# Optimization experiments

Measured on AMD Instinct MI355X. Metric: run time of the kernel, lower is better.

Reference implementation:

```python
import jax, jax.numpy as jnp
import numpy as np

N_HEADS = 8
HEAD_DIM = 64  # hidden_dim 512 / 8 heads
EPS = 1e-12    # F.normalize clamp_min eps


def setup_inputs() -> dict:
    key = jax.random.key(0)
    k1, k2, k3, k4 = jax.random.split(key, 4)
    B, C, H, W = 2, 256, 48, 48
    hidden = N_HEADS * HEAD_DIM
    x = jax.random.normal(k1, (B, C, H, W), dtype=jnp.float32)
    w_qkv = jax.random.normal(k2, (hidden * 3, C), dtype=jnp.float32) * 0.02
    w_proj = jax.random.normal(k3, (C, hidden), dtype=jnp.float32) * 0.02
    b_proj = jax.random.normal(k4, (C,), dtype=jnp.float32) * 0.02
    return {"x": x, "w_qkv": w_qkv, "w_proj": w_proj, "b_proj": b_proj}


def _l2norm_tokens(t):
    # normalize along the token axis (last dim), matching F.normalize(dim=-1)
    n = jnp.sqrt(jnp.sum(t * t, axis=-1, keepdims=True))
    return t / jnp.maximum(n, EPS)


def reference(x, w_qkv, w_proj, b_proj):
    B, C, H, W = x.shape
    N = H * W
    # 1x1 conv == channel matmul
    qkv = jnp.einsum('oc,bchw->bohw', w_qkv, x)  # [B, 3*hidden, H, W]
    qkv = qkv.reshape(B, 3, N_HEADS, HEAD_DIM, N)
    q, k, v = qkv[:, 0], qkv[:, 1], qkv[:, 2]    # each [B, h, d, N]
    q = _l2norm_tokens(q)
    k = _l2norm_tokens(k)
    # attn = q^T @ k over head_dim -> [B, h, N, N]; note: qk_scale unused in source
    attn = jnp.einsum('bhdn,bhdm->bhnm', q, k)
    attn = jax.nn.softmax(attn, axis=-1)
    # out = attn @ v^T -> [B, h, N, d], then permute to [B, h, d, N]
    out = jnp.einsum('bhnm,bhdm->bhdn', attn, v)
    out = out.reshape(B, N_HEADS * HEAD_DIM, H, W)
    # proj 1x1 conv with bias
    y = jnp.einsum('oc,bchw->bohw', w_proj, out) + b_proj[None, :, None, None]
    return y
```

## Files before the change

kernel.cpp:

```cpp
#include <hip/hip_runtime.h>
#include <math.h>

#define NTOK 2304
#define BATCH 2
#define CIN 256
#define HID 512
#define NH 8
#define LOG2E 1.44269504088896340736f

typedef __attribute__((ext_vector_type(8))) short bfrag;
typedef __attribute__((ext_vector_type(16))) float f32x16;

#if __has_builtin(__builtin_amdgcn_exp2f)
#define EXP2(x) __builtin_amdgcn_exp2f(x)
#else
#define EXP2(x) exp2f(x)
#endif

__device__ __forceinline__ unsigned f2bf(float f) {
    unsigned u = __float_as_uint(f);
    u += 0x7FFF + ((u >> 16) & 1);
    return u >> 16;
}

__device__ __forceinline__ unsigned pk_trunc(float a, float b) {
    return __builtin_amdgcn_perm(__float_as_uint(b), __float_as_uint(a), 0x07060302u);
}

__device__ __forceinline__ void softmax_frag(
    const f32x16& accS, int h, float& ps0, float& ps1, bfrag& P0, bfrag& P1)
{
    unsigned dw[8];
#pragma unroll
    for (int i = 0; i < 8; i++) {
        float plo = EXP2(accS[2 * i]);
        float phi = EXP2(accS[2 * i + 1]);
        dw[i] = pk_trunc(plo, phi);
        ps0 += __uint_as_float(dw[i] << 16);
        ps1 += __uint_as_float(dw[i] & 0xffff0000u);
    }
    unsigned sa0 = h ? dw[0] : dw[2], sb0 = h ? dw[1] : dw[3];
    unsigned sa1 = h ? dw[4] : dw[6], sb1 = h ? dw[5] : dw[7];
    unsigned ra0 = (unsigned)__shfl_xor((int)sa0, 32, 64);
    unsigned rb0 = (unsigned)__shfl_xor((int)sb0, 32, 64);
    unsigned ra1 = (unsigned)__shfl_xor((int)sa1, 32, 64);
    unsigned rb1 = (unsigned)__shfl_xor((int)sb1, 32, 64);
    union { bfrag f; unsigned u[4]; } U0, U1;
    U0.u[0] = h ? ra0 : dw[0];  U0.u[1] = h ? rb0 : dw[1];
    U0.u[2] = h ? dw[2] : ra0;  U0.u[3] = h ? dw[3] : rb0;
    U1.u[0] = h ? ra1 : dw[4];  U1.u[1] = h ? rb1 : dw[5];
    U1.u[2] = h ? dw[6] : ra1;  U1.u[3] = h ? dw[7] : rb1;
    P0 = U0.f; P1 = U1.f;
}

__global__ __launch_bounds__(256) void pack_weights(
    const float* __restrict__ wq, short* __restrict__ wqb,
    const float* __restrict__ wp, short* __restrict__ wpb,
    float* __restrict__ sumsq)
{
    if (blockIdx.x == 0) {
        ((float4*)sumsq)[threadIdx.x * 2] = make_float4(0.f, 0.f, 0.f, 0.f);
        ((float4*)sumsq)[threadIdx.x * 2 + 1] = make_float4(0.f, 0.f, 0.f, 0.f);
    }
    int e = (blockIdx.x * 256 + threadIdx.x) * 8;
    const int NQ = 1536 * 256;
    const float* src; short* dst;
    if (e < NQ) {
        int row = e >> 8, c = e & 255;
        int off = (((row >> 5) * 16 + (c >> 4)) * 64 + ((c >> 3) & 1) * 32 + (row & 31)) * 8;
        src = wq + e; dst = wqb + off;
    } else {
        int e2 = e - NQ;
        int row = e2 >> 9, c = e2 & 511;
        int off = (((row >> 5) * 32 + (c >> 4)) * 64 + ((c >> 3) & 1) * 32 + (row & 31)) * 8;
        src = wp + e2; dst = wpb + off;
    }
    float4 v0 = ((const float4*)src)[0];
    float4 v1 = ((const float4*)src)[1];
    unsigned b0 = f2bf(v0.x) | (f2bf(v0.y) << 16);
    unsigned b1 = f2bf(v0.z) | (f2bf(v0.w) << 16);
    unsigned b2 = f2bf(v1.x) | (f2bf(v1.y) << 16);
    unsigned b3 = f2bf(v1.z) | (f2bf(v1.w) << 16);
    *((uint4*)dst) = make_uint4(b0, b1, b2, b3);
}

__global__ __launch_bounds__(256) void pack_xT(
    const float* __restrict__ x, short* __restrict__ xT)
{
    int n0 = blockIdx.x * 64, c0 = blockIdx.y * 64, b = blockIdx.z;
    __shared__ float sT[64][65];
    int tid = threadIdx.x, lane = tid & 63, wv = tid >> 6;
    for (int c = wv; c < 64; c += 4)
        sT[c][lane] = x[((size_t)b * CIN + c0 + c) * NTOK + n0 + lane];
    __syncthreads();
    int n = tid >> 2, c4 = (tid & 3) * 16;
    unsigned buf[8];
#pragma unroll
    for (int i = 0; i < 8; i++)
        buf[i] = f2bf(sT[c4 + 2 * i][n]) | (f2bf(sT[c4 + 2 * i + 1][n]) << 16);
    int n_tok = n0 + n;
    int l31n = n & 31;
    short* dst = xT + (((size_t)b * 72 + (n_tok >> 5)) * 16 + ((c0 + c4) >> 4)) * 512;
    ((uint4*)(dst + (0 * 32 + l31n) * 8))[0] = make_uint4(buf[0], buf[1], buf[2], buf[3]);
    ((uint4*)(dst + (1 * 32 + l31n) * 8))[0] = make_uint4(buf[4], buf[5], buf[6], buf[7]);
}

__global__ __launch_bounds__(256, 2) void gemm_qkv(
    const short* __restrict__ A,
    const short* __restrict__ B,
    short* __restrict__ qku,
    short* __restrict__ vb,
    float* __restrict__ sumsq)
{
    int b = blockIdx.z;
    int o0 = blockIdx.y * 128;
    int n0 = blockIdx.x * 128;
    int tid = threadIdx.x, wv = tid >> 6, lane = tid & 63;
    int h = lane >> 5, l31 = lane & 31;

    const short* pa = A + ((size_t)(o0 >> 5) * 16) * 512 + lane * 8;
    const short* pb = B + (((size_t)b * 72 + (n0 >> 5) + wv) * 16) * 512 + lane * 8;

    f32x16 acc[4];
#pragma unroll
    for (int rb = 0; rb < 4; rb++)
#pragma unroll
        for (int r = 0; r < 16; r++) acc[rb][r] = 0.f;

#pragma unroll 2
    for (int kc = 0; kc < 16; kc++) {
        bfrag a0 = *(const bfrag*)(pa + (size_t)(0 * 16 + kc) * 512);
        bfrag a1 = *(const bfrag*)(pa + (size_t)(1 * 16 + kc) * 512);
        bfrag a2 = *(const bfrag*)(pa + (size_t)(2 * 16 + kc) * 512);
        bfrag a3 = *(const bfrag*)(pa + (size_t)(3 * 16 + kc) * 512);
        bfrag bb = *(const bfrag*)(pb + (size_t)kc * 512);
        acc[0] = __builtin_amdgcn_mfma_f32_32x32x16_bf16(a0, bb, acc[0], 0, 0, 0);
        acc[1] = __builtin_amdgcn_mfma_f32_32x32x16_bf16(a1, bb, acc[1], 0, 0, 0);
        acc[2] = __builtin_amdgcn_mfma_f32_32x32x16_bf16(a2, bb, acc[2], 0, 0, 0);
        acc[3] = __builtin_amdgcn_mfma_f32_32x32x16_bf16(a3, bb, acc[3], 0, 0, 0);
    }

    int nn = n0 + wv * 32 + l31;
    if (o0 < 1024) {
        int sel = o0 >> 9;
        short* Qb = qku + (size_t)sel * (16 * NTOK * 64);
        int mbase = (nn >> 5) * 4, tl = nn & 31;
#pragma unroll
        for (int rb = 0; rb < 4; rb++)
#pragma unroll
            for (int r = 0; r < 16; r++) {
                int ml = (r & 3) + 8 * (r >> 2) + 4 * h;
                int o = o0 + rb * 32 + ml;
                int hh2 = (o >> 6) & 7, d = o & 63;
                float v = acc[rb][r];
                float sq = v * v;
#pragma unroll
                for (int off = 1; off < 32; off <<= 1)
                    sq += __shfl_xor(sq, off, 64);
                if (l31 == 0)
                    atomicAdd(sumsq + b * 1024 + o, sq);
                Qb[(size_t)(b * 8 + hh2) * (NTOK * 64)
                   + (size_t)(mbase + (d >> 4)) * 512
                   + (((d >> 3) & 1) * 32 + tl) * 8 + (d & 7)] = (short)f2bf(v);
            }
    } else {
        short* V = vb + (size_t)b * 512 * NTOK;
        int ov = o0 - 1024;
        int mb = nn >> 5, jc = (nn >> 4) & 1, hv = (nn >> 3) & 1, e = nn & 7;
#pragma unroll
        for (int rb = 0; rb < 4; rb++)
#pragma unroll
            for (int r = 0; r < 16; r++) {
                int ml = (r & 3) + 8 * (r >> 2) + 4 * h;
                int row = ov + rb * 32 + ml;
                int hh2 = row >> 6, dl = row & 63;
                int jr = dl >> 5, l31v = dl & 31;
                V[((((size_t)hh2 * 72 + mb) * 4 + jr * 2 + jc) * 64
                   + hv * 32 + l31v) * 8 + e] = (short)f2bf(acc[rb][r]);
            }
    }
}

__global__ __launch_bounds__(256) void scale_qk(
    short* __restrict__ qkt, const float* __restrict__ sumsq)
{
    int s = blockIdx.x * 256 + threadIdx.x;
    int lane = s & 63;
    int rest = s >> 6;
    int fi = rest & 3;
    int selbh = rest / 288;
    int sel = selbh >> 4, bh = selbh & 15;
    int b = bh >> 3, hh = bh & 7;
    int d0 = fi * 16 + (lane >> 5) * 8;
    const float* sp = sumsq + b * 1024 + sel * 512 + hh * 64 + d0;
    float scl = sel == 0 ? LOG2E : 1.f;
    float4 s0 = ((const float4*)sp)[0];
    float4 s1 = ((const float4*)sp)[1];
    float i0 = scl / fmaxf(sqrtf(s0.x), 1e-12f);
    float i1 = scl / fmaxf(sqrtf(s0.y), 1e-12f);
    float i2 = scl / fmaxf(sqrtf(s0.z), 1e-12f);
    float i3 = scl / fmaxf(sqrtf(s0.w), 1e-12f);
    float i4 = scl / fmaxf(sqrtf(s1.x), 1e-12f);
    float i5 = scl / fmaxf(sqrtf(s1.y), 1e-12f);
    float i6 = scl / fmaxf(sqrtf(s1.z), 1e-12f);
    float i7 = scl / fmaxf(sqrtf(s1.w), 1e-12f);
    uint4 v = ((uint4*)qkt)[s];
    unsigned o0w = f2bf(__uint_as_float(v.x << 16) * i0)
                 | (f2bf(__uint_as_float(v.x & 0xffff0000u) * i1) << 16);
    unsigned o1w = f2bf(__uint_as_float(v.y << 16) * i2)
                 | (f2bf(__uint_as_float(v.y & 0xffff0000u) * i3) << 16);
    unsigned o2w = f2bf(__uint_as_float(v.z << 16) * i4)
                 | (f2bf(__uint_as_float(v.z & 0xffff0000u) * i5) << 16);
    unsigned o3w = f2bf(__uint_as_float(v.w << 16) * i6)
                 | (f2bf(__uint_as_float(v.w & 0xffff0000u) * i7) << 16);
    ((uint4*)qkt)[s] = make_uint4(o0w, o1w, o2w, o3w);
}

__global__ __launch_bounds__(256, 4) void attn_nb(
    const short* __restrict__ qkt,
    const short* __restrict__ vb,
    short* __restrict__ Opart,
    float* __restrict__ lsum)
{
    int bid = blockIdx.x;
    int g = bid & 63;
    int bh = g >> 2, ms = g & 3;
    int ntile = bid >> 6;
    int b = bh >> 3, hh = bh & 7;
    int tid = threadIdx.x, wv = tid >> 6, lane = tid & 63;
    int h = lane >> 5, l31 = lane & 31;
    int nb = ntile * 128 + wv * 32;
    int mb0 = ms * 18;

    const short* Qt = qkt + (size_t)bh * NTOK * 64;
    const short* kp = qkt + (size_t)16 * NTOK * 64 + (size_t)bh * NTOK * 64
                    + ((size_t)mb0 * 4) * 512 + lane * 8;
    const short* vp = vb + (((size_t)(b * 8 + hh) * 72 + mb0) * 4) * 512 + lane * 8;

    bfrag bQ[4];
    {
        const short* q0 = Qt + ((size_t)(nb >> 5) * 4) * 512 + lane * 8;
#pragma unroll
        for (int i = 0; i < 4; i++) bQ[i] = *(const bfrag*)(q0 + i * 512);
    }

    f32x16 aL, aH;
#pragma unroll
    for (int r = 0; r < 16; r++) { aL[r] = 0.f; aH[r] = 0.f; }
    float s0 = 0.f, s1 = 0.f;

    bfrag ck[4], cv[4];
#pragma unroll
    for (int i = 0; i < 4; i++) {
        ck[i] = *(const bfrag*)(kp + i * 512);
        cv[i] = *(const bfrag*)(vp + i * 512);
    }

#pragma unroll 2
    for (int it = 0; it < 18; it++) {
        kp += 2048; vp += 2048;
        bfrag nk[4], nv[4];
#pragma unroll
        for (int i = 0; i < 4; i++) {
            nk[i] = *(const bfrag*)(kp + i * 512);
            nv[i] = *(const bfrag*)(vp + i * 512);
        }

        bfrag P0, P1;
        {
            f32x16 accS;
#pragma unroll
            for (int r = 0; r < 16; r++) accS[r] = 0.f;
            accS = __builtin_amdgcn_mfma_f32_32x32x16_bf16(ck[0], bQ[0], accS, 0, 0, 0);
            accS = __builtin_amdgcn_mfma_f32_32x32x16_bf16(ck[1], bQ[1], accS, 0, 0, 0);
            accS = __builtin_amdgcn_mfma_f32_32x32x16_bf16(ck[2], bQ[2], accS, 0, 0, 0);
            accS = __builtin_amdgcn_mfma_f32_32x32x16_bf16(ck[3], bQ[3], accS, 0, 0, 0);
            softmax_frag(accS, h, s0, s1, P0, P1);
        }
        aL = __builtin_amdgcn_mfma_f32_32x32x16_bf16(P0, cv[0], aL, 0, 0, 0);
        aL = __builtin_amdgcn_mfma_f32_32x32x16_bf16(P1, cv[1], aL, 0, 0, 0);
        aH = __builtin_amdgcn_mfma_f32_32x32x16_bf16(P0, cv[2], aH, 0, 0, 0);
        aH = __builtin_amdgcn_mfma_f32_32x32x16_bf16(P1, cv[3], aH, 0, 0, 0);

#pragma unroll
        for (int i = 0; i < 4; i++) { ck[i] = nk[i]; cv[i] = nv[i]; }
    }

    float p0 = s0 + s1;
    p0 += __shfl_xor(p0, 32, 64);
    if (h == 0)
        lsum[((size_t)ms * 16 + bh) * NTOK + nb + l31] = p0;

    short* Ob = Opart + (size_t)ms * (2ull * NTOK * HID)
              + (size_t)b * NTOK * HID + hh * 64;
#pragma unroll
    for (int r = 0; r < 16; r++) {
        int ml = (r & 3) + 8 * (r >> 2) + 4 * h;
        Ob[(size_t)(nb + ml) * HID + l31] = (short)f2bf(aL[r]);
        Ob[(size_t)(nb + ml) * HID + 32 + l31] = (short)f2bf(aH[r]);
    }
}

__global__ __launch_bounds__(256) void combine(
    const short* __restrict__ Opart, const float* __restrict__ lsum,
    short* __restrict__ aoT)
{
    int s = blockIdx.x * 256 + threadIdx.x;
    int lane = s & 63, kc = (s >> 6) & 31, nbb = s >> 11;
    int b = nbb >= 72 ? 1 : 0, nb = nbb - 72 * b;
    int h = lane >> 5, l31 = lane & 31;
    int n = nb * 32 + l31;
    int k0 = kc * 16 + h * 8;
    int hh = kc >> 2;
    float l = 0.f;
#pragma unroll
    for (int ms = 0; ms < 4; ms++)
        l += lsum[((size_t)ms * 16 + b * 8 + hh) * NTOK + n];
    float inv = 1.f / l;
    float a[8] = {0.f, 0.f, 0.f, 0.f, 0.f, 0.f, 0.f, 0.f};
#pragma unroll
    for (int ms = 0; ms < 4; ms++) {
        const short* P = Opart + (size_t)ms * (2ull * NTOK * HID)
                       + ((size_t)b * NTOK + n) * HID + k0;
        uint4 v = *(const uint4*)P;
        a[0] += __uint_as_float(v.x << 16);
        a[1] += __uint_as_float(v.x & 0xffff0000u);
        a[2] += __uint_as_float(v.y << 16);
        a[3] += __uint_as_float(v.y & 0xffff0000u);
        a[4] += __uint_as_float(v.z << 16);
        a[5] += __uint_as_float(v.z & 0xffff0000u);
        a[6] += __uint_as_float(v.w << 16);
        a[7] += __uint_as_float(v.w & 0xffff0000u);
    }
    unsigned b0 = f2bf(a[0] * inv) | (f2bf(a[1] * inv) << 16);
    unsigned b1 = f2bf(a[2] * inv) | (f2bf(a[3] * inv) << 16);
    unsigned b2 = f2bf(a[4] * inv) | (f2bf(a[5] * inv) << 16);
    unsigned b3 = f2bf(a[6] * inv) | (f2bf(a[7] * inv) << 16);
    *((uint4*)(aoT + (size_t)s * 8)) = make_uint4(b0, b1, b2, b3);
}

__global__ __launch_bounds__(256, 2) void gemm_proj(
    const short* __restrict__ A,
    const short* __restrict__ B,
    const float* __restrict__ bias, float* __restrict__ y)
{
    int b = blockIdx.z;
    int o0 = blockIdx.y * 64;
    int n0 = blockIdx.x * 128;
    int tid = threadIdx.x, wv = tid >> 6, lane = tid & 63;
    int h = lane >> 5, l31 = lane & 31;

    const short* pa = A + ((size_t)(o0 >> 5) * 32) * 512 + lane * 8;
    const short* pb = B + (((size_t)b * 72 + (n0 >> 5) + wv) * 32) * 512 + lane * 8;

    f32x16 acc0, acc1;
#pragma unroll
    for (int r = 0; r < 16; r++) { acc0[r] = 0.f; acc1[r] = 0.f; }

#pragma unroll 4
    for (int kc = 0; kc < 32; kc++) {
        bfrag a0 = *(const bfrag*)(pa + (size_t)kc * 512);
        bfrag a1 = *(const bfrag*)(pa + (size_t)(32 + kc) * 512);
        bfrag bb = *(const bfrag*)(pb + (size_t)kc * 512);
        acc0 = __builtin_amdgcn_mfma_f32_32x32x16_bf16(a0, bb, acc0, 0, 0, 0);
        acc1 = __builtin_amdgcn_mfma_f32_32x32x16_bf16(a1, bb, acc1, 0, 0, 0);
    }

    int nn = n0 + wv * 32 + l31;
#pragma unroll
    for (int r = 0; r < 16; r++) {
        int ml = (r & 3) + 8 * (r >> 2) + 4 * h;
        y[((size_t)b * CIN + o0 + ml) * NTOK + nn] = acc0[r] + bias[o0 + ml];
        y[((size_t)b * CIN + o0 + 32 + ml) * NTOK + nn] = acc1[r] + bias[o0 + 32 + ml];
    }
}

extern "C" void kernel_launch(void* const* d_in, const int* in_sizes, int n_in,
                              void* d_out, int out_size, void* d_ws, size_t ws_size,
                              hipStream_t stream)
{
    const float* x      = (const float*)d_in[0];
    const float* w_qkv  = (const float*)d_in[1];
    const float* w_proj = (const float*)d_in[2];
    const float* b_proj = (const float*)d_in[3];
    float* y = (float*)d_out;

    short* Opart = (short*)d_ws;
    short* vb    = (short*)((char*)d_ws + 18874368);
    short* qkt   = (short*)((char*)d_ws + 23592960);
    short* aoT   = (short*)((char*)d_ws + 23592960);
    float* lsum  = (float*)((char*)d_ws + 33030144);
    short* xT    = (short*)((char*)d_ws + 33030144);
    short* wqb   = (short*)((char*)d_ws + 35389440);
    short* wpb   = (short*)((char*)d_ws + 36175872);
    float* sumsq = (float*)((char*)d_ws + 36438016);

    pack_weights<<<(1536 * 256 + 256 * 512) / 8 / 256, 256, 0, stream>>>(
        w_qkv, wqb, w_proj, wpb, sumsq);
    pack_xT<<<dim3(NTOK / 64, CIN / 64, BATCH), 256, 0, stream>>>(x, xT);
    gemm_qkv<<<dim3(NTOK / 128, 1536 / 128, BATCH), 256, 0, stream>>>(
        wqb, xT, qkt, vb, sumsq);
    scale_qk<<<2304, 256, 0, stream>>>(qkt, sumsq);
    attn_nb<<<1152, 256, 0, stream>>>(qkt, vb, Opart, lsum);
    combine<<<1152, 256, 0, stream>>>(Opart, lsum, aoT);
    gemm_proj<<<dim3(NTOK / 128, CIN / 64, BATCH), 256, 0, stream>>>(
        wpb, aoT, b_proj, y);
}
```

Before: 163.0 us.

## Split sumsq into own kernel, double query tiles per wave, retile Opart layout

Removes the per-element shuffle reduction and atomics from the QKV GEMM epilogue and moves the squared-norm accumulation into a separate sumsq_qk kernel that reads the bf16 q/k buffer. The attention kernel now processes two 32-query tiles per wave with 128-thread blocks, so each K/V fragment load feeds twice the MFMA work at the cost of more accumulator registers. Opart is written in the fragment-tiled layout the combine kernel reads linearly, which simplifies combine's addressing. The softmax row-sum accumulation is rebalanced into a tree to shorten the dependency chain. Norms are now computed from bf16-rounded values instead of fp32, a small numerical change.

```diff
diff --git a/kernel.cpp b/kernel.cpp
--- a/kernel.cpp
+++ b/kernel.cpp
@@ -23,6 +23,10 @@
     return u >> 16;
 }
 
+__device__ __forceinline__ float bf2f(unsigned short s) {
+    return __uint_as_float(((unsigned)s) << 16);
+}
+
 __device__ __forceinline__ unsigned pk_trunc(float a, float b) {
     return __builtin_amdgcn_perm(__float_as_uint(b), __float_as_uint(a), 0x07060302u);
 }
@@ -31,14 +35,17 @@
     const f32x16& accS, int h, float& ps0, float& ps1, bfrag& P0, bfrag& P1)
 {
     unsigned dw[8];
+    float e0[8], e1[8];
 #pragma unroll
     for (int i = 0; i < 8; i++) {
         float plo = EXP2(accS[2 * i]);
         float phi = EXP2(accS[2 * i + 1]);
         dw[i] = pk_trunc(plo, phi);
-        ps0 += __uint_as_float(dw[i] << 16);
-        ps1 += __uint_as_float(dw[i] & 0xffff0000u);
-    }
+        e0[i] = __uint_as_float(dw[i] << 16);
+        e1[i] = __uint_as_float(dw[i] & 0xffff0000u);
+    }
+    ps0 += ((e0[0] + e0[1]) + (e0[2] + e0[3])) + ((e0[4] + e0[5]) + (e0[6] + e0[7]));
+    ps1 += ((e1[0] + e1[1]) + (e1[2] + e1[3])) + ((e1[4] + e1[5]) + (e1[6] + e1[7]));
     unsigned sa0 = h ? dw[0] : dw[2], sb0 = h ? dw[1] : dw[3];
     unsigned sa1 = h ? dw[4] : dw[6], sb1 = h ? dw[5] : dw[7];
     unsigned ra0 = (unsigned)__shfl_xor((int)sa0, 32, 64);
@@ -109,8 +116,7 @@
     const short* __restrict__ A,
     const short* __restrict__ B,
     short* __restrict__ qku,
-    short* __restrict__ vb,
-    float* __restrict__ sumsq)
+    short* __restrict__ vb)
 {
     int b = blockIdx.z;
     int o0 = blockIdx.y * 128;
@@ -152,16 +158,9 @@
                 int ml = (r & 3) + 8 * (r >> 2) + 4 * h;
                 int o = o0 + rb * 32 + ml;
                 int hh2 = (o >> 6) & 7, d = o & 63;
-                float v = acc[rb][r];
-                float sq = v * v;
-#pragma unroll
-                for (int off = 1; off < 32; off <<= 1)
-                    sq += __shfl_xor(sq, off, 64);
-                if (l31 == 0)
-                    atomicAdd(sumsq + b * 1024 + o, sq);
                 Qb[(size_t)(b * 8 + hh2) * (NTOK * 64)
                    + (size_t)(mbase + (d >> 4)) * 512
-                   + (((d >> 3) & 1) * 32 + tl) * 8 + (d & 7)] = (short)f2bf(v);
+                   + (((d >> 3) & 1) * 32 + tl) * 8 + (d & 7)] = (short)f2bf(acc[rb][r]);
             }
     } else {
         short* V = vb + (size_t)b * 512 * NTOK;
@@ -178,6 +177,41 @@
                 V[((((size_t)hh2 * 72 + mb) * 4 + jr * 2 + jc) * 64
                    + hv * 32 + l31v) * 8 + e] = (short)f2bf(acc[rb][r]);
             }
+    }
+}
+
+__global__ __launch_bounds__(64) void sumsq_qk(
+    const short* __restrict__ qkt, float* __restrict__ sumsq)
+{
+    int bid = blockIdx.x;
+    int mc = bid % 9;
+    int rest = bid / 9;
+    int i = rest & 3;
+    int selbh = rest >> 2;
+    int lane = threadIdx.x;
+    const short* p = qkt + (((size_t)selbh * 72 + mc * 8) * 4 + i) * 512 + lane * 8;
+    float sq[8] = {0.f, 0.f, 0.f, 0.f, 0.f, 0.f, 0.f, 0.f};
+#pragma unroll
+    for (int m = 0; m < 8; m++) {
+        bfrag v = *(const bfrag*)(p + (size_t)m * 2048);
+#pragma unroll
+        for (int e = 0; e < 8; e++) {
+            float f = bf2f((unsigned short)v[e]);
+            sq[e] += f * f;
+        }
+    }
+#pragma unroll
+    for (int off = 1; off <= 16; off <<= 1)
+#pragma unroll
+        for (int e = 0; e < 8; e++)
+            sq[e] += __shfl_xor(sq[e], off, 64);
+    if ((lane & 31) == 0) {
+        int sel = selbh >> 4, bh = selbh & 15;
+        int b = bh >> 3, hh = bh & 7, hsel = lane >> 5;
+        int dbase = i * 16 + hsel * 8;
+        float* dst = sumsq + b * 1024 + sel * 512 + hh * 64 + dbase;
+#pragma unroll
+        for (int e = 0; e < 8; e++) atomicAdd(dst + e, sq[e]);
     }
 }
 
@@ -216,7 +250,7 @@
     ((uint4*)qkt)[s] = make_uint4(o0w, o1w, o2w, o3w);
 }
 
-__global__ __launch_bounds__(256, 4) void attn_nb(
+__global__ __launch_bounds__(128, 2) void attn_nb(
     const short* __restrict__ qkt,
     const short* __restrict__ vb,
     short* __restrict__ Opart,
@@ -229,7 +263,8 @@
     int b = bh >> 3, hh = bh & 7;
     int tid = threadIdx.x, wv = tid >> 6, lane = tid & 63;
     int h = lane >> 5, l31 = lane & 31;
-    int nb = ntile * 128 + wv * 32;
+    int nb0 = ntile * 128 + wv * 32;
+    int nb1 = nb0 + 64;
     int mb0 = ms * 18;
 
     const short* Qt = qkt + (size_t)bh * NTOK * 64;
@@ -237,17 +272,21 @@
                     + ((size_t)mb0 * 4) * 512 + lane * 8;
     const short* vp = vb + (((size_t)(b * 8 + hh) * 72 + mb0) * 4) * 512 + lane * 8;
 
-    bfrag bQ[4];
+    bfrag bQ0[4], bQ1[4];
     {
-        const short* q0 = Qt + ((size_t)(nb >> 5) * 4) * 512 + lane * 8;
-#pragma unroll
-        for (int i = 0; i < 4; i++) bQ[i] = *(const bfrag*)(q0 + i * 512);
-    }
-
-    f32x16 aL, aH;
-#pragma unroll
-    for (int r = 0; r < 16; r++) { aL[r] = 0.f; aH[r] = 0.f; }
-    float s0 = 0.f, s1 = 0.f;
+        const short* q0 = Qt + ((size_t)(nb0 >> 5) * 4) * 512 + lane * 8;
+        const short* q1 = Qt + ((size_t)(nb1 >> 5) * 4) * 512 + lane * 8;
+#pragma unroll
+        for (int i = 0; i < 4; i++) {
+            bQ0[i] = *(const bfrag*)(q0 + i * 512);
+            bQ1[i] = *(const bfrag*)(q1 + i * 512);
+        }
+    }
+
+    f32x16 aL0, aH0, aL1, aH1;
+#pragma unroll
+    for (int r = 0; r < 16; r++) { aL0[r] = 0.f; aH0[r] = 0.f; aL1[r] = 0.f; aH1[r] = 0.f; }
+    float s00 = 0.f, s01 = 0.f, s10 = 0.f, s11 = 0.f;
 
     bfrag ck[4], cv[4];
 #pragma unroll
@@ -266,38 +305,63 @@
             nv[i] = *(const bfrag*)(vp + i * 512);
         }
 
-        bfrag P0, P1;
+        bfrag P00, P01, P10, P11;
         {
             f32x16 accS;
 #pragma unroll
             for (int r = 0; r < 16; r++) accS[r] = 0.f;
-            accS = __builtin_amdgcn_mfma_f32_32x32x16_bf16(ck[0], bQ[0], accS, 0, 0, 0);
-            accS = __builtin_amdgcn_mfma_f32_32x32x16_bf16(ck[1], bQ[1], accS, 0, 0, 0);
-            accS = __builtin_amdgcn_mfma_f32_32x32x16_bf16(ck[2], bQ[2], accS, 0, 0, 0);
-            accS = __builtin_amdgcn_mfma_f32_32x32x16_bf16(ck[3], bQ[3], accS, 0, 0, 0);
-            softmax_frag(accS, h, s0, s1, P0, P1);
+            accS = __builtin_amdgcn_mfma_f32_32x32x16_bf16(ck[0], bQ0[0], accS, 0, 0, 0);
+            accS = __builtin_amdgcn_mfma_f32_32x32x16_bf16(ck[1], bQ0[1], accS, 0, 0, 0);
+            accS = __builtin_amdgcn_mfma_f32_32x32x16_bf16(ck[2], bQ0[2], accS, 0, 0, 0);
+            accS = __builtin_amdgcn_mfma_f32_32x32x16_bf16(ck[3], bQ0[3], accS, 0, 0, 0);
+            softmax_frag(accS, h, s00, s01, P00, P01);
         }
-        aL = __builtin_amdgcn_mfma_f32_32x32x16_bf16(P0, cv[0], aL, 0, 0, 0);
-        aL = __builtin_amdgcn_mfma_f32_32x32x16_bf16(P1, cv[1], aL, 0, 0, 0);
-        aH = __builtin_amdgcn_mfma_f32_32x32x16_bf16(P0, cv[2], aH, 0, 0, 0);
-        aH = __builtin_amdgcn_mfma_f32_32x32x16_bf16(P1, cv[3], aH, 0, 0, 0);
+        {
+            f32x16 accS;
+#pragma unroll
+            for (int r = 0; r < 16; r++) accS[r] = 0.f;
+            accS = __builtin_amdgcn_mfma_f32_32x32x16_bf16(ck[0], bQ1[0], accS, 0, 0, 0);
+            accS = __builtin_amdgcn_mfma_f32_32x32x16_bf16(ck[1], bQ1[1], accS, 0, 0, 0);
+            accS = __builtin_amdgcn_mfma_f32_32x32x16_bf16(ck[2], bQ1[2], accS, 0, 0, 0);
+            accS = __builtin_amdgcn_mfma_f32_32x32x16_bf16(ck[3], bQ1[3], accS, 0, 0, 0);
+            softmax_frag(accS, h, s10, s11, P10, P11);
+        }
+        aL0 = __builtin_amdgcn_mfma_f32_32x32x16_bf16(P00, cv[0], aL0, 0, 0, 0);
+        aL0 = __builtin_amdgcn_mfma_f32_32x32x16_bf16(P01, cv[1], aL0, 0, 0, 0);
+        aH0 = __builtin_amdgcn_mfma_f32_32x32x16_bf16(P00, cv[2], aH0, 0, 0, 0);
+        aH0 = __builtin_amdgcn_mfma_f32_32x32x16_bf16(P01, cv[3], aH0, 0, 0, 0);
+        aL1 = __builtin_amdgcn_mfma_f32_32x32x16_bf16(P10, cv[0], aL1, 0, 0, 0);
+        aL1 = __builtin_amdgcn_mfma_f32_32x32x16_bf16(P11, cv[1], aL1, 0, 0, 0);
+        aH1 = __builtin_amdgcn_mfma_f32_32x32x16_bf16(P10, cv[2], aH1, 0, 0, 0);
+        aH1 = __builtin_amdgcn_mfma_f32_32x32x16_bf16(P11, cv[3], aH1, 0, 0, 0);
 
 #pragma unroll
         for (int i = 0; i < 4; i++) { ck[i] = nk[i]; cv[i] = nv[i]; }
     }
 
-    float p0 = s0 + s1;
+    float p0 = s00 + s01;
     p0 += __shfl_xor(p0, 32, 64);
-    if (h == 0)
-        lsum[((size_t)ms * 16 + bh) * NTOK + nb + l31] = p0;
-
-    short* Ob = Opart + (size_t)ms * (2ull * NTOK * HID)
-              + (size_t)b * NTOK * HID + hh * 64;
+    float p1 = s10 + s11;
+    p1 += __shfl_xor(p1, 32, 64);
+    if (h == 0) {
+        lsum[((size_t)ms * 16 + bh) * NTOK + nb0 + l31] = p0;
+        lsum[((size_t)ms * 16 + bh) * NTOK + nb1 + l31] = p1;
+    }
+
+    short* Ob = Opart + ((size_t)ms * 2 + b) * (72 * 32 * 64 * 8);
+    int nbs0 = nb0 >> 5, nbs1 = nb1 >> 5;
+    int kcL = hh * 4 + (l31 >> 4);
+    int kcH = kcL + 2;
+    int e = l31 & 7;
+    int hs8 = ((l31 >> 3) & 1) * 32;
 #pragma unroll
     for (int r = 0; r < 16; r++) {
         int ml = (r & 3) + 8 * (r >> 2) + 4 * h;
-        Ob[(size_t)(nb + ml) * HID + l31] = (short)f2bf(aL[r]);
-        Ob[(size_t)(nb + ml) * HID + 32 + l31] = (short)f2bf(aH[r]);
+        int wi = hs8 + ml;
+        Ob[(((size_t)nbs0 * 32 + kcL) * 64 + wi) * 8 + e] = (short)f2bf(aL0[r]);
+        Ob[(((size_t)nbs0 * 32 + kcH) * 64 + wi) * 8 + e] = (short)f2bf(aH0[r]);
+        Ob[(((size_t)nbs1 * 32 + kcL) * 64 + wi) * 8 + e] = (short)f2bf(aL1[r]);
+        Ob[(((size_t)nbs1 * 32 + kcH) * 64 + wi) * 8 + e] = (short)f2bf(aH1[r]);
     }
 }
 
@@ -308,21 +372,19 @@
     int s = blockIdx.x * 256 + threadIdx.x;
     int lane = s & 63, kc = (s >> 6) & 31, nbb = s >> 11;
     int b = nbb >= 72 ? 1 : 0, nb = nbb - 72 * b;
-    int h = lane >> 5, l31 = lane & 31;
+    int l31 = lane & 31;
     int n = nb * 32 + l31;
-    int k0 = kc * 16 + h * 8;
     int hh = kc >> 2;
     float l = 0.f;
 #pragma unroll
     for (int ms = 0; ms < 4; ms++)
         l += lsum[((size_t)ms * 16 + b * 8 + hh) * NTOK + n];
     float inv = 1.f / l;
+    const size_t MS = 2ull * 72 * 32 * 64 * 8;
     float a[8] = {0.f, 0.f, 0.f, 0.f, 0.f, 0.f, 0.f, 0.f};
 #pragma unroll
     for (int ms = 0; ms < 4; ms++) {
-        const short* P = Opart + (size_t)ms * (2ull * NTOK * HID)
-                       + ((size_t)b * NTOK + n) * HID + k0;
-        uint4 v = *(const uint4*)P;
+        uint4 v = *(const uint4*)(Opart + (size_t)ms * MS + (size_t)s * 8);
         a[0] += __uint_as_float(v.x << 16);
         a[1] += __uint_as_float(v.x & 0xffff0000u);
         a[2] += __uint_as_float(v.y << 16);
@@ -399,9 +461,10 @@
         w_qkv, wqb, w_proj, wpb, sumsq);
     pack_xT<<<dim3(NTOK / 64, CIN / 64, BATCH), 256, 0, stream>>>(x, xT);
     gemm_qkv<<<dim3(NTOK / 128, 1536 / 128, BATCH), 256, 0, stream>>>(
-        wqb, xT, qkt, vb, sumsq);
+        wqb, xT, qkt, vb);
+    sumsq_qk<<<1152, 64, 0, stream>>>(qkt, sumsq);
     scale_qk<<<2304, 256, 0, stream>>>(qkt, sumsq);
-    attn_nb<<<1152, 256, 0, stream>>>(qkt, vb, Opart, lsum);
+    attn_nb<<<1152, 128, 0, stream>>>(qkt, vb, Opart, lsum);
     combine<<<1152, 256, 0, stream>>>(Opart, lsum, aoT);
     gemm_proj<<<dim3(NTOK / 128, CIN / 64, BATCH), 256, 0, stream>>>(
         wpb, aoT, b_proj, y);
```

New measurement: 143.8 us. -11.8%, faster.
